# Kernel optimization log

Measured on AMD Instinct MI355X. Metric: run time of the kernel, lower is better.

The kernel has to match this reference:

```python
import jax, jax.numpy as jnp
import numpy as np

MIXTURE_COUNT = 4
GAUSSIANS_PER_MIXTURE = 4
EM_ITERS = 3
EPS = 1e-4


def setup_inputs() -> dict:
    key = jax.random.key(0)
    k1, k2 = jax.random.split(key)
    B, C, N = 1, 3, 1048576
    input_tensor = jax.random.normal(k1, (B, C, N), dtype=jnp.float32)
    label_tensor = jax.random.randint(k2, (B, N), 0, MIXTURE_COUNT, dtype=jnp.int32)
    return {"input_tensor": input_tensor, "label_tensor": label_tensor}


def _gmm_em(x, mix_oh, M, G):
    # x: [B,N,C] features, mix_oh: [B,N,M] one-hot mixture labels
    B, N, C = x.shape
    eye = jnp.eye(C, dtype=x.dtype)
    # init: split each mixture's pixels round-robin across its G gaussians
    sub_oh = jax.nn.one_hot(jnp.arange(N) % G, G, dtype=x.dtype)  # [N,G]
    resp = mix_oh[:, :, :, None] * sub_oh[None, :, None, :]       # [B,N,M,G]
    logp = None
    for _ in range(EM_ITERS):
        # ---- M-step: label-segmented weighted stats ----
        w = resp.sum(axis=1) + EPS                                 # [B,M,G]
        mu = jnp.einsum('bnmg,bnc->bmgc', resp, x) / w[..., None]  # [B,M,G,C]
        xx = jnp.einsum('bnmg,bnc,bnd->bmgcd', resp, x, x) / w[..., None, None]
        cov = xx - mu[..., :, None] * mu[..., None, :] + EPS * eye  # [B,M,G,C,C]
        prec = jnp.linalg.inv(cov)
        _, logdet = jnp.linalg.slogdet(cov)                        # [B,M,G]
        pi = w / w.sum(axis=2, keepdims=True)                      # [B,M,G]
        # ---- E-step: per-pixel Gaussian log-likelihoods ----
        # Mahalanobis via expansion to avoid [B,N,M,G,C] residual tensor
        xPx = jnp.einsum('bnc,bmgcd,bnd->bnmg', x, prec, x)
        xPm = jnp.einsum('bnc,bmgcd,bmgd->bnmg', x, prec, mu)
        mPm = jnp.einsum('bmgc,bmgcd,bmgd->bmg', mu, prec, mu)
        quad = xPx - 2.0 * xPm + mPm[:, None]                      # [B,N,M,G]
        logp = (jnp.log(pi)[:, None]
                - 0.5 * (quad + logdet[:, None] + C * jnp.log(2.0 * jnp.pi)))
        # pixels only redistribute among the gaussians of their own mixture
        resp = mix_oh[..., None] * jax.nn.softmax(logp, axis=3)
    return logp


def reference(input_tensor, label_tensor):
    M, G = MIXTURE_COUNT, GAUSSIANS_PER_MIXTURE
    x = jnp.swapaxes(input_tensor, 1, 2)                           # [B,N,C]
    mix_oh = jax.nn.one_hot(label_tensor, M, dtype=x.dtype)        # [B,N,M]
    logp = _gmm_em(x, mix_oh, M, G)                                # [B,N,M,G]
    # posterior over mixtures for every pixel
    mix_log = jax.nn.logsumexp(logp, axis=3)                       # [B,N,M]
    post = jax.nn.softmax(mix_log, axis=2)
    return jnp.swapaxes(post, 1, 2)                                # [B,M,N]
```

## Files before the change

kernel.cpp:

```cpp
#include <hip/hip_runtime.h>
#include <math.h>


#define NTHR  256
#define NBLK  512
#define EPS_F 1e-4f
#define LOG2PI3 5.5136311992280366f


static __device__ void compute_params(const float* __restrict__ sumsIn,
                                      float* spar, float* sums, float* wtab,
                                      int tid) {
    if (tid < 160) {
        float4 v = ((const float4*)sumsIn)[tid];
        sums[tid] = (v.x + v.y) + (v.z + v.w);
    }
    __syncthreads();
    if (tid < 16) wtab[tid] = sums[tid * 10] + EPS_F;
    __syncthreads();
    if (tid < 16) {
        const int tt = tid;
        const float* S = &sums[tt * 10];
        const float w  = wtab[tt];
        const float iw = 1.0f / w;
        float mu0 = S[1] * iw, mu1 = S[2] * iw, mu2 = S[3] * iw;
        float c00 = S[4] * iw - mu0 * mu0 + EPS_F;
        float c01 = S[5] * iw - mu0 * mu1;
        float c02 = S[6] * iw - mu0 * mu2;
        float c11 = S[7] * iw - mu1 * mu1 + EPS_F;
        float c12 = S[8] * iw - mu1 * mu2;
        float c22 = S[9] * iw - mu2 * mu2 + EPS_F;
        float d00 = c11 * c22 - c12 * c12;
        float d01 = c02 * c12 - c01 * c22;
        float d02 = c01 * c12 - c02 * c11;
        float det = c00 * d00 + c01 * d01 + c02 * d02;
        float idet = 1.0f / det;
        float P00 = d00 * idet, P01 = d01 * idet, P02 = d02 * idet;
        float P11 = (c00 * c22 - c02 * c02) * idet;
        float P12 = (c01 * c02 - c00 * c12) * idet;
        float P22 = (c00 * c11 - c01 * c01) * idet;
        float logdet = logf(det);
        const int mb = tt & 12;
        float wsum = wtab[mb] + wtab[mb + 1] + wtab[mb + 2] + wtab[mb + 3];
        float logpi = logf(w) - logf(wsum);
        float pm0 = P00 * mu0 + P01 * mu1 + P02 * mu2;
        float pm1 = P01 * mu0 + P11 * mu1 + P12 * mu2;
        float pm2 = P02 * mu0 + P12 * mu1 + P22 * mu2;
        float mPm = mu0 * pm0 + mu1 * pm1 + mu2 * pm2;
        float c0 = logpi - 0.5f * (mPm + logdet + LOG2PI3);
        float* P = spar + tt * 12;
        P[0] = pm0; P[1] = pm1; P[2] = pm2; P[3] = c0;
        P[4] = -0.5f * P00; P[5] = -0.5f * P11; P[6] = -0.5f * P22;
        P[7] = -P01; P[8] = -P02; P[9] = -P12;
        P[10] = 0.f; P[11] = 0.f;
    }
    __syncthreads();
}

__global__ __launch_bounds__(NTHR, 2) void k_accum(const float* __restrict__ x,
                                                   const int* __restrict__ lab,
                                                   const float* __restrict__ sumsIn,
                                                   float* __restrict__ sumsOut,
                                                   int N, int mode) {
    __shared__ __align__(16) float spar[192];
    __shared__ float sums[160];
    __shared__ float wtab[16];
    __shared__ float sred[NTHR / 64][160];
    const int tid  = threadIdx.x;
    const int wave = tid >> 6, lane = tid & 63;
    const int q    = lane & 3;
    const int qb   = lane & ~3;
    if (mode) compute_params(sumsIn, spar, sums, wtab, tid);

    float acc[40];
    #pragma unroll
    for (int k = 0; k < 40; ++k) acc[k] = 0.f;

    const int groups = N >> 2;
    const int stride = gridDim.x * NTHR;
    const int gid    = blockIdx.x * NTHR + tid;
    const int trips  = (groups + stride - 1) / stride;
    const float4* x0p = (const float4*)x;
    const float4* x1p = (const float4*)(x + N);
    const float4* x2p = (const float4*)(x + 2 * N);
    const int4*   lp  = (const int4*)lab;

    for (int tr = 0; tr < trips; ++tr) {
        const int i  = tr * stride + gid;
        const bool valid = i < groups;
        const int ii = valid ? i : 0;
        float4 va = x0p[ii], vb = x1p[ii], vc = x2p[ii];
        int4   m4 = lp[ii];
        float pa[4] = {va.x, va.y, va.z, va.w};
        float pb[4] = {vb.x, vb.y, vb.z, vb.w};
        float pc[4] = {vc.x, vc.y, vc.z, vc.w};
        int   pm[4] = {m4.x, m4.y, m4.z, m4.w};
        if (!valid) { pm[0] = pm[1] = pm[2] = pm[3] = -1; }

        #pragma unroll
        for (int j = 0; j < 4; ++j) {
            const float a = pa[j], b = pb[j], c = pc[j];
            const int   m = pm[j];
            float ws[4] = {0.f, 0.f, 0.f, 0.f};
            if (mode) {
                const float* P0 = spar + (m & 3) * 48;
                float l[4];
                #pragma unroll
                for (int g = 0; g < 4; ++g) {
                    const float* P = P0 + g * 12;
                    float4 q0 = *(const float4*)(P);
                    float4 q1 = *(const float4*)(P + 4);
                    float2 q2 = *(const float2*)(P + 8);
                    l[g] = q0.w + q0.x * a + q0.y * b + q0.z * c
                         + q1.x * (a * a) + q1.y * (b * b) + q1.z * (c * c)
                         + q1.w * (a * b) + q2.x * (a * c) + q2.y * (b * c);
                }
                float mx = fmaxf(fmaxf(l[0], l[1]), fmaxf(l[2], l[3]));
                float e0 = __expf(l[0] - mx), e1 = __expf(l[1] - mx);
                float e2 = __expf(l[2] - mx), e3 = __expf(l[3] - mx);
                float rs = 1.0f / (e0 + e1 + e2 + e3);
                ws[0] = e0 * rs; ws[1] = e1 * rs; ws[2] = e2 * rs; ws[3] = e3 * rs;
            }
            #pragma unroll
            for (int src = 0; src < 4; ++src) {
                const float ra = __shfl(a, qb + src, 64);
                const float rb = __shfl(b, qb + src, 64);
                const float rc = __shfl(c, qb + src, 64);
                const int   rm = __shfl(m, qb + src, 64);
                const bool sel = (rm == q);
                const float aa = ra * ra, ab = ra * rb, ac = ra * rc;
                const float bb = rb * rb, bc = rb * rc, cc = rc * rc;
                if (mode) {
                    float rw[4];
                    rw[0] = __shfl(ws[0], qb + src, 64);
                    rw[1] = __shfl(ws[1], qb + src, 64);
                    rw[2] = __shfl(ws[2], qb + src, 64);
                    rw[3] = __shfl(ws[3], qb + src, 64);
                    #pragma unroll
                    for (int g = 0; g < 4; ++g) {
                        const float s = sel ? rw[g] : 0.f;
                        float* A = &acc[g * 10];
                        A[0] += s;
                        A[1] = fmaf(s, ra, A[1]);
                        A[2] = fmaf(s, rb, A[2]);
                        A[3] = fmaf(s, rc, A[3]);
                        A[4] = fmaf(s, aa, A[4]);
                        A[5] = fmaf(s, ab, A[5]);
                        A[6] = fmaf(s, ac, A[6]);
                        A[7] = fmaf(s, bb, A[7]);
                        A[8] = fmaf(s, bc, A[8]);
                        A[9] = fmaf(s, cc, A[9]);
                    }
                } else {
                    const float s = sel ? 1.f : 0.f;
                    float* A = &acc[j * 10];
                    A[0] += s;
                    A[1] = fmaf(s, ra, A[1]);
                    A[2] = fmaf(s, rb, A[2]);
                    A[3] = fmaf(s, rc, A[3]);
                    A[4] = fmaf(s, aa, A[4]);
                    A[5] = fmaf(s, ab, A[5]);
                    A[6] = fmaf(s, ac, A[6]);
                    A[7] = fmaf(s, bb, A[7]);
                    A[8] = fmaf(s, bc, A[8]);
                    A[9] = fmaf(s, cc, A[9]);
                }
            }
        }
    }

    #pragma unroll
    for (int k = 0; k < 40; ++k) {
        float v = acc[k];
        v += __shfl_xor(v,  4, 64);
        v += __shfl_xor(v,  8, 64);
        v += __shfl_xor(v, 16, 64);
        v += __shfl_xor(v, 32, 64);
        acc[k] = v;
    }
    if (lane < 4) {
        #pragma unroll
        for (int k = 0; k < 40; ++k) sred[wave][lane * 40 + k] = acc[k];
    }
    __syncthreads();
    if (tid < 160) {
        float s = sred[0][tid] + sred[1][tid] + sred[2][tid] + sred[3][tid];
        unsafeAtomicAdd(&sumsOut[tid * 4 + (blockIdx.x & 3)], s);
    }
}

__global__ __launch_bounds__(NTHR, 2) void k_final(const float* __restrict__ x,
                                                   const float* __restrict__ sumsIn,
                                                   float* __restrict__ out,
                                                   int N) {
    __shared__ __align__(16) float spar[192];
    __shared__ float sums[160];
    __shared__ float wtab[16];
    compute_params(sumsIn, spar, sums, wtab, threadIdx.x);
    const int lane = threadIdx.x & 63;
    const int q    = lane & 3;
    const int qb   = lane & ~3;
    float PR[40];
    #pragma unroll
    for (int g = 0; g < 4; ++g)
        #pragma unroll
        for (int k = 0; k < 10; ++k) PR[g * 10 + k] = spar[q * 48 + g * 12 + k];

    const int groups = N >> 2;
    const int stride = gridDim.x * NTHR;
    const int gid    = blockIdx.x * NTHR + threadIdx.x;
    const int trips  = (groups + stride - 1) / stride;
    const float4* x0p = (const float4*)x;
    const float4* x1p = (const float4*)(x + N);
    const float4* x2p = (const float4*)(x + 2 * N);

    for (int tr = 0; tr < trips; ++tr) {
        const int i  = tr * stride + gid;
        const bool valid = i < groups;
        const int ii = valid ? i : 0;
        float4 va = x0p[ii], vb = x1p[ii], vc = x2p[ii];
        float pa[4] = {va.x, va.y, va.z, va.w};
        float pb[4] = {vb.x, vb.y, vb.z, vb.w};
        float pc[4] = {vc.x, vc.y, vc.z, vc.w};
        float po[4][4];

        #pragma unroll
        for (int j = 0; j < 4; ++j) {
            const float a = pa[j], b = pb[j], c = pc[j];
            float M[4];
            #pragma unroll
            for (int p = 0; p < 4; ++p) {
                const float ra = __shfl(a, qb + p, 64);
                const float rb = __shfl(b, qb + p, 64);
                const float rc = __shfl(c, qb + p, 64);
                const float aa = ra * ra, ab = ra * rb, ac = ra * rc;
                const float bb = rb * rb, bc = rb * rc, cc = rc * rc;
                float l[4];
                #pragma unroll
                for (int g = 0; g < 4; ++g) {
                    const float* P = &PR[g * 10];
                    l[g] = P[3] + P[0] * ra + P[1] * rb + P[2] * rc
                         + P[4] * aa + P[5] * bb + P[6] * cc
                         + P[7] * ab + P[8] * ac + P[9] * bc;
                }
                float mx = fmaxf(fmaxf(l[0], l[1]), fmaxf(l[2], l[3]));
                M[p] = mx + __logf(__expf(l[0] - mx) + __expf(l[1] - mx)
                                 + __expf(l[2] - mx) + __expf(l[3] - mx));
            }
            float W[4] = {0.f, 0.f, 0.f, 0.f};
            #pragma unroll
            for (int k = 0; k < 4; ++k) {
                #pragma unroll
                for (int qq = 0; qq < 4; ++qq) {
                    float v = __shfl(M[k], qb + qq, 64);
                    if (q == k) W[qq] = v;
                }
            }
            float mmx = fmaxf(fmaxf(W[0], W[1]), fmaxf(W[2], W[3]));
            float e0 = __expf(W[0] - mmx), e1 = __expf(W[1] - mmx);
            float e2 = __expf(W[2] - mmx), e3 = __expf(W[3] - mmx);
            float rs = 1.0f / (e0 + e1 + e2 + e3);
            po[j][0] = e0 * rs; po[j][1] = e1 * rs;
            po[j][2] = e2 * rs; po[j][3] = e3 * rs;
        }
        if (valid) {
            #pragma unroll
            for (int m = 0; m < 4; ++m) {
                ((float4*)(out + (size_t)m * N))[i] =
                    make_float4(po[0][m], po[1][m], po[2][m], po[3][m]);
            }
        }
    }
}

extern "C" void kernel_launch(void* const* d_in, const int* in_sizes, int n_in,
                              void* d_out, int out_size, void* d_ws, size_t ws_size,
                              hipStream_t stream) {
    const float* x   = (const float*)d_in[0];
    const int*   lab = (const int*)d_in[1];
    float* out = (float*)d_out;
    const int N = in_sizes[1];

    float* sums = (float*)d_ws;
    hipMemsetAsync(sums, 0, 3 * 640 * sizeof(float), stream);

    dim3 grid(NBLK), blk(NTHR);
    k_accum<<<grid, blk, 0, stream>>>(x, lab, sums, sums, N, 0);
    k_accum<<<grid, blk, 0, stream>>>(x, lab, sums, sums + 640, N, 1);
    k_accum<<<grid, blk, 0, stream>>>(x, lab, sums + 640, sums + 1280, N, 1);
    k_final<<<grid, blk, 0, stream>>>(x, sums + 1280, out, N);
}
```

Measured before the change: 151.6 us.

## Use DPP lane moves, template mode, widen atomic banks, double grid and occupancy

Replaces the 4-lane-group __shfl broadcasts with DPP quad_perm moves and the first two xor-shuffle reduction steps with DPP row shifts, which avoids LDS-routed bpermute traffic. The runtime mode flag becomes a template parameter so each specialisation drops dead branches. The grid doubles to 1024 blocks, launch bounds allow 4 blocks per CU, and partial-sum atomics spread over 8 banks instead of 4 to cut contention. The higher occupancy target may force register spills given the 40-float accumulators.

After: 235.1 us. 1.55x slower.

```diff
diff --git a/kernel.cpp b/kernel.cpp
--- a/kernel.cpp
+++ b/kernel.cpp
@@ -3,17 +3,30 @@
 
 
 #define NTHR  256
-#define NBLK  512
+#define NBLK  1024
+#define NBANK 8
 #define EPS_F 1e-4f
 #define LOG2PI3 5.5136311992280366f
+
+template<int CTRL>
+__device__ __forceinline__ float dpp_f(float v) {
+    return __int_as_float(
+        __builtin_amdgcn_mov_dpp(__float_as_int(v), CTRL, 0xF, 0xF, false));
+}
+template<int CTRL>
+__device__ __forceinline__ int dpp_i(int v) {
+    return __builtin_amdgcn_mov_dpp(v, CTRL, 0xF, 0xF, false);
+}
 
 
 static __device__ void compute_params(const float* __restrict__ sumsIn,
                                       float* spar, float* sums, float* wtab,
                                       int tid) {
     if (tid < 160) {
-        float4 v = ((const float4*)sumsIn)[tid];
-        sums[tid] = (v.x + v.y) + (v.z + v.w);
+        float4 v0 = ((const float4*)sumsIn)[tid * 2];
+        float4 v1 = ((const float4*)sumsIn)[tid * 2 + 1];
+        sums[tid] = ((v0.x + v0.y) + (v0.z + v0.w))
+                  + ((v1.x + v1.y) + (v1.z + v1.w));
     }
     __syncthreads();
     if (tid < 16) wtab[tid] = sums[tid * 10] + EPS_F;
@@ -57,11 +70,49 @@
     __syncthreads();
 }
 
-__global__ __launch_bounds__(NTHR, 2) void k_accum(const float* __restrict__ x,
+#define ACC10(APTR, S)                                                      \
+    {   float* A = (APTR);                                                  \
+        A[0] += (S);                                                        \
+        A[1] = fmaf((S), ra, A[1]);                                         \
+        A[2] = fmaf((S), rb, A[2]);                                         \
+        A[3] = fmaf((S), rc, A[3]);                                         \
+        A[4] = fmaf((S), aa, A[4]);                                         \
+        A[5] = fmaf((S), ab, A[5]);                                         \
+        A[6] = fmaf((S), ac, A[6]);                                         \
+        A[7] = fmaf((S), bb, A[7]);                                         \
+        A[8] = fmaf((S), bc, A[8]);                                         \
+        A[9] = fmaf((S), cc, A[9]);                                         }
+
+#define SRC_STEP(SRC_)                                                      \
+    {   const float ra = dpp_f<(SRC_) * 0x55>(a);                           \
+        const float rb = dpp_f<(SRC_) * 0x55>(b);                           \
+        const float rc = dpp_f<(SRC_) * 0x55>(c);                           \
+        const int   rm = dpp_i<(SRC_) * 0x55>(m);                           \
+        const bool sel = (rm == q);                                         \
+        const float aa = ra * ra, ab = ra * rb, ac = ra * rc;               \
+        const float bb = rb * rb, bc = rb * rc, cc = rc * rc;               \
+        if (MODE) {                                                         \
+            const float rw0 = dpp_f<(SRC_) * 0x55>(ws0);                    \
+            const float rw1 = dpp_f<(SRC_) * 0x55>(ws1);                    \
+            const float rw2 = dpp_f<(SRC_) * 0x55>(ws2);                    \
+            const float rw3 = dpp_f<(SRC_) * 0x55>(ws3);                    \
+            { const float s = sel ? rw0 : 0.f; ACC10(&acc[0],  s) }         \
+            { const float s = sel ? rw1 : 0.f; ACC10(&acc[10], s) }         \
+            { const float s = sel ? rw2 : 0.f; ACC10(&acc[20], s) }         \
+            { const float s = sel ? rw3 : 0.f; ACC10(&acc[30], s) }         \
+        } else {                                                            \
+                                     \
+            const float s = sel ? 1.f : 0.f;                                \
+            ACC10(&acc[j * 10], s)                                          \
+        }                                                                   \
+    }
+
+template<int MODE>
+__global__ __launch_bounds__(NTHR, 4) void k_accum(const float* __restrict__ x,
                                                    const int* __restrict__ lab,
                                                    const float* __restrict__ sumsIn,
                                                    float* __restrict__ sumsOut,
-                                                   int N, int mode) {
+                                                   int N) {
     __shared__ __align__(16) float spar[192];
     __shared__ float sums[160];
     __shared__ float wtab[16];
@@ -69,8 +120,7 @@
     const int tid  = threadIdx.x;
     const int wave = tid >> 6, lane = tid & 63;
     const int q    = lane & 3;
-    const int qb   = lane & ~3;
-    if (mode) compute_params(sumsIn, spar, sums, wtab, tid);
+    if (MODE) compute_params(sumsIn, spar, sums, wtab, tid);
 
     float acc[40];
     #pragma unroll
@@ -101,8 +151,8 @@
         for (int j = 0; j < 4; ++j) {
             const float a = pa[j], b = pb[j], c = pc[j];
             const int   m = pm[j];
-            float ws[4] = {0.f, 0.f, 0.f, 0.f};
-            if (mode) {
+            float ws0 = 0.f, ws1 = 0.f, ws2 = 0.f, ws3 = 0.f;
+            if (MODE) {
                 const float* P0 = spar + (m & 3) * 48;
                 float l[4];
                 #pragma unroll
@@ -119,61 +169,17 @@
                 float e0 = __expf(l[0] - mx), e1 = __expf(l[1] - mx);
                 float e2 = __expf(l[2] - mx), e3 = __expf(l[3] - mx);
                 float rs = 1.0f / (e0 + e1 + e2 + e3);
-                ws[0] = e0 * rs; ws[1] = e1 * rs; ws[2] = e2 * rs; ws[3] = e3 * rs;
+                ws0 = e0 * rs; ws1 = e1 * rs; ws2 = e2 * rs; ws3 = e3 * rs;
             }
-            #pragma unroll
-            for (int src = 0; src < 4; ++src) {
-                const float ra = __shfl(a, qb + src, 64);
-                const float rb = __shfl(b, qb + src, 64);
-                const float rc = __shfl(c, qb + src, 64);
-                const int   rm = __shfl(m, qb + src, 64);
-                const bool sel = (rm == q);
-                const float aa = ra * ra, ab = ra * rb, ac = ra * rc;
-                const float bb = rb * rb, bc = rb * rc, cc = rc * rc;
-                if (mode) {
-                    float rw[4];
-                    rw[0] = __shfl(ws[0], qb + src, 64);
-                    rw[1] = __shfl(ws[1], qb + src, 64);
-                    rw[2] = __shfl(ws[2], qb + src, 64);
-                    rw[3] = __shfl(ws[3], qb + src, 64);
-                    #pragma unroll
-                    for (int g = 0; g < 4; ++g) {
-                        const float s = sel ? rw[g] : 0.f;
-                        float* A = &acc[g * 10];
-                        A[0] += s;
-                        A[1] = fmaf(s, ra, A[1]);
-                        A[2] = fmaf(s, rb, A[2]);
-                        A[3] = fmaf(s, rc, A[3]);
-                        A[4] = fmaf(s, aa, A[4]);
-                        A[5] = fmaf(s, ab, A[5]);
-                        A[6] = fmaf(s, ac, A[6]);
-                        A[7] = fmaf(s, bb, A[7]);
-                        A[8] = fmaf(s, bc, A[8]);
-                        A[9] = fmaf(s, cc, A[9]);
-                    }
-                } else {
-                    const float s = sel ? 1.f : 0.f;
-                    float* A = &acc[j * 10];
-                    A[0] += s;
-                    A[1] = fmaf(s, ra, A[1]);
-                    A[2] = fmaf(s, rb, A[2]);
-                    A[3] = fmaf(s, rc, A[3]);
-                    A[4] = fmaf(s, aa, A[4]);
-                    A[5] = fmaf(s, ab, A[5]);
-                    A[6] = fmaf(s, ac, A[6]);
-                    A[7] = fmaf(s, bb, A[7]);
-                    A[8] = fmaf(s, bc, A[8]);
-                    A[9] = fmaf(s, cc, A[9]);
-                }
-            }
+            SRC_STEP(0) SRC_STEP(1) SRC_STEP(2) SRC_STEP(3)
         }
     }
 
     #pragma unroll
     for (int k = 0; k < 40; ++k) {
         float v = acc[k];
-        v += __shfl_xor(v,  4, 64);
-        v += __shfl_xor(v,  8, 64);
+        v += dpp_f<0x124>(v);
+        v += dpp_f<0x128>(v);
         v += __shfl_xor(v, 16, 64);
         v += __shfl_xor(v, 32, 64);
         acc[k] = v;
@@ -185,11 +191,11 @@
     __syncthreads();
     if (tid < 160) {
         float s = sred[0][tid] + sred[1][tid] + sred[2][tid] + sred[3][tid];
-        unsafeAtomicAdd(&sumsOut[tid * 4 + (blockIdx.x & 3)], s);
-    }
-}
-
-__global__ __launch_bounds__(NTHR, 2) void k_final(const float* __restrict__ x,
+        unsafeAtomicAdd(&sumsOut[tid * NBANK + (blockIdx.x & (NBANK - 1))], s);
+    }
+}
+
+__global__ __launch_bounds__(NTHR, 4) void k_final(const float* __restrict__ x,
                                                    const float* __restrict__ sumsIn,
                                                    float* __restrict__ out,
                                                    int N) {
@@ -199,7 +205,6 @@
     compute_params(sumsIn, spar, sums, wtab, threadIdx.x);
     const int lane = threadIdx.x & 63;
     const int q    = lane & 3;
-    const int qb   = lane & ~3;
     float PR[40];
     #pragma unroll
     for (int g = 0; g < 4; ++g)
@@ -213,6 +218,29 @@
     const float4* x0p = (const float4*)x;
     const float4* x1p = (const float4*)(x + N);
     const float4* x2p = (const float4*)(x + 2 * N);
+
+#define FIN_P(P_)                                                           \
+    {   const float ra = dpp_f<(P_) * 0x55>(a);                             \
+        const float rb = dpp_f<(P_) * 0x55>(b);                             \
+        const float rc = dpp_f<(P_) * 0x55>(c);                             \
+        const float aa = ra * ra, ab = ra * rb, ac = ra * rc;               \
+        const float bb = rb * rb, bc = rb * rc, cc = rc * rc;               \
+        float l[4];                                                         \
+        _Pragma("unroll")                                                   \
+        for (int g = 0; g < 4; ++g) {                                       \
+            const float* P = &PR[g * 10];                                   \
+            l[g] = P[3] + P[0] * ra + P[1] * rb + P[2] * rc                 \
+                 + P[4] * aa + P[5] * bb + P[6] * cc                        \
+                 + P[7] * ab + P[8] * ac + P[9] * bc;                       \
+        }                                                                   \
+        float mx = fmaxf(fmaxf(l[0], l[1]), fmaxf(l[2], l[3]));             \
+        M[P_] = mx + __logf(__expf(l[0] - mx) + __expf(l[1] - mx)          \
+                          + __expf(l[2] - mx) + __expf(l[3] - mx));         \
+    }
+
+#define TRS(K_, QQ_)                                                        \
+    {   const float v = dpp_f<(QQ_) * 0x55>(M[K_]);                         \
+        if (q == (K_)) W[QQ_] = v;                                          }
 
     for (int tr = 0; tr < trips; ++tr) {
         const int i  = tr * stride + gid;
@@ -228,34 +256,12 @@
         for (int j = 0; j < 4; ++j) {
             const float a = pa[j], b = pb[j], c = pc[j];
             float M[4];
-            #pragma unroll
-            for (int p = 0; p < 4; ++p) {
-                const float ra = __shfl(a, qb + p, 64);
-                const float rb = __shfl(b, qb + p, 64);
-                const float rc = __shfl(c, qb + p, 64);
-                const float aa = ra * ra, ab = ra * rb, ac = ra * rc;
-                const float bb = rb * rb, bc = rb * rc, cc = rc * rc;
-                float l[4];
-                #pragma unroll
-                for (int g = 0; g < 4; ++g) {
-                    const float* P = &PR[g * 10];
-                    l[g] = P[3] + P[0] * ra + P[1] * rb + P[2] * rc
-                         + P[4] * aa + P[5] * bb + P[6] * cc
-                         + P[7] * ab + P[8] * ac + P[9] * bc;
-                }
-                float mx = fmaxf(fmaxf(l[0], l[1]), fmaxf(l[2], l[3]));
-                M[p] = mx + __logf(__expf(l[0] - mx) + __expf(l[1] - mx)
-                                 + __expf(l[2] - mx) + __expf(l[3] - mx));
-            }
+            FIN_P(0) FIN_P(1) FIN_P(2) FIN_P(3)
             float W[4] = {0.f, 0.f, 0.f, 0.f};
-            #pragma unroll
-            for (int k = 0; k < 4; ++k) {
-                #pragma unroll
-                for (int qq = 0; qq < 4; ++qq) {
-                    float v = __shfl(M[k], qb + qq, 64);
-                    if (q == k) W[qq] = v;
-                }
-            }
+            TRS(0, 0) TRS(0, 1) TRS(0, 2) TRS(0, 3)
+            TRS(1, 0) TRS(1, 1) TRS(1, 2) TRS(1, 3)
+            TRS(2, 0) TRS(2, 1) TRS(2, 2) TRS(2, 3)
+            TRS(3, 0) TRS(3, 1) TRS(3, 2) TRS(3, 3)
             float mmx = fmaxf(fmaxf(W[0], W[1]), fmaxf(W[2], W[3]));
             float e0 = __expf(W[0] - mmx), e1 = __expf(W[1] - mmx);
             float e2 = __expf(W[2] - mmx), e3 = __expf(W[3] - mmx);
@@ -282,11 +288,11 @@
     const int N = in_sizes[1];
 
     float* sums = (float*)d_ws;
-    hipMemsetAsync(sums, 0, 3 * 640 * sizeof(float), stream);
+    hipMemsetAsync(sums, 0, 3 * 160 * NBANK * sizeof(float), stream);
 
     dim3 grid(NBLK), blk(NTHR);
-    k_accum<<<grid, blk, 0, stream>>>(x, lab, sums, sums, N, 0);
-    k_accum<<<grid, blk, 0, stream>>>(x, lab, sums, sums + 640, N, 1);
-    k_accum<<<grid, blk, 0, stream>>>(x, lab, sums + 640, sums + 1280, N, 1);
-    k_final<<<grid, blk, 0, stream>>>(x, sums + 1280, out, N);
-}
+    k_accum<0><<<grid, blk, 0, stream>>>(x, lab, sums, sums, N);
+    k_accum<1><<<grid, blk, 0, stream>>>(x, lab, sums, sums + 1280, N);
+    k_accum<1><<<grid, blk, 0, stream>>>(x, lab, sums + 1280, sums + 2560, N);
+    k_final<<<grid, blk, 0, stream>>>(x, sums + 2560, out, N);
+}
```
